# Kernel optimization log

Measured on AMD Instinct MI355X. Metric: run time of the kernel, lower is better.

## Reference

```python
import jax, jax.numpy as jnp
import numpy as np

B, N, D, H = 16, 512, 256, 8
DK = D // H
EPS = 1e-6
NEG_INF = 1e12
LAM_ATT, LAM_DIST, LAM_ADJ = 0.3, 0.3, 0.4


def setup_inputs() -> dict:
    key = jax.random.key(0)
    ks = jax.random.split(key, 16)
    inp = {
        "query": jax.random.normal(ks[0], (B, N, D), jnp.float32),
        "key": jax.random.normal(ks[1], (B, N, D), jnp.float32),
        "value": jax.random.normal(ks[2], (B, N, D), jnp.float32),
        "adj_matrix": jax.random.uniform(ks[3], (B, N, N), jnp.float32),
        "distances_matrix": jax.random.uniform(ks[4], (B, N, N), jnp.float32),
        "edges_att": jnp.zeros((1,), jnp.float32),
        "mask": jnp.ones((B, N), jnp.int32),
    }
    s = 1.0 / np.sqrt(D)
    # four Linear(d_model, d_model): Wq, Wk, Wv, Wo (+ biases)
    for i, nm in enumerate(["q", "k", "v", "o"]):
        inp[f"W{nm}"] = jax.random.normal(ks[5 + 2 * i], (D, D), jnp.float32) * s
        inp[f"b{nm}"] = jax.random.normal(ks[6 + 2 * i], (D,), jnp.float32) * s
    return inp


def _proj(x, W, b):
    # [B,N,D] -> [B,H,N,DK]
    y = x @ W.T + b
    return y.reshape(B, N, H, DK).transpose(0, 2, 1, 3)


def reference(query, key, value, adj_matrix, distances_matrix, edges_att, mask,
              Wq, bq, Wk, bk, Wv, bv, Wo, bo):
    q = _proj(query, Wq, bq)
    k = _proj(key, Wk, bk)
    v = _proj(value, Wv, bv)

    valid = mask != 0  # [B,N] key-side validity

    # distance kernel: softmax(-d) over keys, masked positions -> 0 prob
    d_scores = jnp.where(valid[:, None, :], -distances_matrix, -jnp.inf)
    p_dist = jax.nn.softmax(d_scores, axis=-1)  # [B,N,N]

    # scaled dot-product attention with key mask
    scores = jnp.einsum("bhqd,bhkd->bhqk", q, k) / np.sqrt(DK)
    scores = jnp.where(valid[:, None, None, :], scores, -NEG_INF)
    p_attn = jax.nn.softmax(scores, axis=-1)  # [B,H,N,N]

    # row-normalized adjacency
    p_adj = adj_matrix / (adj_matrix.sum(axis=-1, keepdims=True) + EPS)  # [B,N,N]

    # blend three attention terms (broadcast dist/adj over heads)
    p_weighted = (LAM_ATT * p_attn
                  + LAM_DIST * p_dist[:, None]
                  + LAM_ADJ * p_adj[:, None])  # [B,H,N,N]

    x = jnp.einsum("bhqk,bhkd->bhqd", p_weighted, v)  # [B,H,N,DK]
    x = x.transpose(0, 2, 1, 3).reshape(B, N, D)
    out = x @ Wo.T + bo  # output projection (4th linear)
    return out
```

## Files before the change

### kernel.cpp

```cpp
#include <hip/hip_runtime.h>
#include <cstdint>
#include <cstddef>

#define B_  16
#define N_  512
#define D_  256
#define H_  8
#define DK_ 32

#define QKV_ELEMS 2097152

__device__ __align__(16) unsigned short g_Qb[QKV_ELEMS];
__device__ __align__(16) unsigned short g_Kb[QKV_ELEMS];
__device__ __align__(16) unsigned short g_VT[QKV_ELEMS];
__device__ __align__(16) unsigned short g_WoB[D_*D_];

typedef short v8s __attribute__((ext_vector_type(8)));
typedef float v4f __attribute__((ext_vector_type(4)));

__device__ __forceinline__ unsigned short f2b(float f){
  unsigned int x;
  __builtin_memcpy(&x, &f, 4);
  x = x + 0x7FFFu + ((x >> 16) & 1u);
  return (unsigned short)(x >> 16);
}
__device__ __forceinline__ v8s pack8(const float4 a, const float4 b){
  v8s o;
  o[0]=(short)f2b(a.x); o[1]=(short)f2b(a.y); o[2]=(short)f2b(a.z); o[3]=(short)f2b(a.w);
  o[4]=(short)f2b(b.x); o[5]=(short)f2b(b.y); o[6]=(short)f2b(b.z); o[7]=(short)f2b(b.w);
  return o;
}

__global__ __launch_bounds__(256) void fused_pre(
    const float* __restrict__ query, const float* __restrict__ key_,
    const float* __restrict__ value,
    const float* __restrict__ Wq, const float* __restrict__ bq,
    const float* __restrict__ Wk, const float* __restrict__ bk,
    const float* __restrict__ Wv, const float* __restrict__ bv,
    const float* __restrict__ Wo)
{
  __shared__ unsigned short Wl[64*264];
  const int bid = blockIdx.x;
  const int t   = threadIdx.x;

  if (bid >= 1536){
    const int i = ((bid - 1536)*256 + t)*4;
    const float4 u = *reinterpret_cast<const float4*>(Wo + i);
    ushort4 o4;
    o4.x = f2b(u.x); o4.y = f2b(u.y); o4.z = f2b(u.z); o4.w = f2b(u.w);
    *reinterpret_cast<ushort4*>(g_WoB + i) = o4;
    return;
  }

  const int z  = bid >> 9;
  const int rr = bid & 511;
  const int mt = rr >> 2, nt = rr & 3;
  const float* Ap = (z==0) ? query : (z==1) ? key_ : value;
  const float* Wp = (z==0) ? Wq : (z==1) ? Wk : Wv;
  const float* bp = (z==0) ? bq : (z==1) ? bk : bv;
  const int w = t >> 6, lane = t & 63, kl = lane & 15, quad = lane >> 4;
  const int m0 = mt*64 + w*16;
  const int n0 = nt*64;

  {
    const int row = t >> 2;
    const int ks  = (t & 3) * 64;
    const float* src = Wp + (size_t)(n0+row)*256 + ks;
    unsigned short* dst = Wl + row*264 + ks;
    #pragma unroll
    for (int u = 0; u < 8; ++u){
      const float4 u0 = reinterpret_cast<const float4*>(src)[2*u];
      const float4 u1 = reinterpret_cast<const float4*>(src)[2*u+1];
      *reinterpret_cast<v8s*>(dst + u*8) = pack8(u0, u1);
    }
  }
  __syncthreads();

  v4f acc[4];
  #pragma unroll
  for (int nb = 0; nb < 4; ++nb) acc[nb] = (v4f){0.f,0.f,0.f,0.f};
  const int arow = m0 + kl;

  if (z == 2){
    #pragma unroll
    for (int k0 = 0; k0 < 256; k0 += 32){
      const float* ap = Ap + (size_t)arow*256 + k0 + quad*8;
      const v8s af = pack8(reinterpret_cast<const float4*>(ap)[0],
                           reinterpret_cast<const float4*>(ap)[1]);
      #pragma unroll
      for (int nb = 0; nb < 4; ++nb){
        const v8s wf = *reinterpret_cast<const v8s*>(&Wl[(nb*16+kl)*264 + k0 + quad*8]);
        acc[nb] = __builtin_amdgcn_mfma_f32_16x16x32_bf16(wf, af, acc[nb], 0, 0, 0);
      }
    }
    const int tok = m0 + kl, bb = tok >> 9, nr = tok & 511;
    #pragma unroll
    for (int nb = 0; nb < 4; ++nb)
      #pragma unroll
      for (int r = 0; r < 4; ++r){
        const int n = n0 + nb*16 + quad*4 + r;
        const float v = acc[nb][r] + bp[n];
        g_VT[(((size_t)bb*H_ + (n>>5))*DK_ + (n&31))*N_ + nr] = f2b(v);
      }
  } else {
    #pragma unroll
    for (int k0 = 0; k0 < 256; k0 += 32){
      const float* ap = Ap + (size_t)arow*256 + k0 + quad*8;
      const v8s af = pack8(reinterpret_cast<const float4*>(ap)[0],
                           reinterpret_cast<const float4*>(ap)[1]);
      #pragma unroll
      for (int nb = 0; nb < 4; ++nb){
        const v8s wf = *reinterpret_cast<const v8s*>(&Wl[(nb*16+kl)*264 + k0 + quad*8]);
        acc[nb] = __builtin_amdgcn_mfma_f32_16x16x32_bf16(af, wf, acc[nb], 0, 0, 0);
      }
    }
    unsigned short* dst = z ? g_Kb : g_Qb;
    #pragma unroll
    for (int nb = 0; nb < 4; ++nb){
      const int n = n0 + nb*16 + kl;
      const float bias = bp[n];
      #pragma unroll
      for (int r = 0; r < 4; ++r){
        const int m = m0 + quad*4 + r;
        const float v = acc[nb][r] + bias;
        dst[(((size_t)(m>>9)*H_ + (n>>5))*N_ + (m&511))*DK_ + (n&31)] = f2b(v);
      }
    }
  }
}

__global__ __launch_bounds__(512) void attn_kernel(
    const float* __restrict__ dist, const float* __restrict__ adjm,
    const int* __restrict__ mask,   const float* __restrict__ bo,
    float* __restrict__ out)
{
  __shared__ unsigned short STl[16*520];
  __shared__ unsigned short Pl[8*16*40];
  __shared__ unsigned short Xl[16*272];
  const int bid = blockIdx.x;
  const int b  = bid & 15;
  const int qt = bid >> 4;
  const int q0 = qt*16;
  const int t  = threadIdx.x;
  const int w  = t >> 6, lane = t & 63;
  const int kl = lane & 15, quad = lane >> 4;

  {
    const int row = t >> 5;
    const int seg = t & 31;
    const size_t roff = ((size_t)(b*N_ + q0 + row))*N_ + seg*16;
    float dv[16], av[16]; int mk[16];
    #pragma unroll
    for (int c = 0; c < 4; ++c){
      const float4 d4 = *reinterpret_cast<const float4*>(dist + roff + c*4);
      const float4 a4 = *reinterpret_cast<const float4*>(adjm + roff + c*4);
      const int4   m4 = *reinterpret_cast<const int4*>(mask + b*N_ + seg*16 + c*4);
      dv[c*4+0]=d4.x; dv[c*4+1]=d4.y; dv[c*4+2]=d4.z; dv[c*4+3]=d4.w;
      av[c*4+0]=a4.x; av[c*4+1]=a4.y; av[c*4+2]=a4.z; av[c*4+3]=a4.w;
      mk[c*4+0]=m4.x; mk[c*4+1]=m4.y; mk[c*4+2]=m4.z; mk[c*4+3]=m4.w;
    }
    float ev[16], lz = 0.f, la = 0.f;
    #pragma unroll
    for (int i = 0; i < 16; ++i){
      ev[i] = mk[i] ? __expf(-dv[i]) : 0.f;
      lz += ev[i];
      la += av[i];
    }
    #pragma unroll
    for (int o = 1; o < 32; o <<= 1){
      lz += __shfl_xor(lz, o, 64);
      la += __shfl_xor(la, o, 64);
    }
    const float c0 = (lz > 0.f) ? 0.3f / lz : 0.f;
    const float c1 = 0.4f / (la + 1e-6f);
    v8s s0, s1;
    #pragma unroll
    for (int i = 0; i < 8; ++i){
      s0[i] = (short)f2b(ev[i]*c0   + av[i]*c1);
      s1[i] = (short)f2b(ev[8+i]*c0 + av[8+i]*c1);
    }
    *reinterpret_cast<v8s*>(&STl[row*520 + seg*16])     = s0;
    *reinterpret_cast<v8s*>(&STl[row*520 + seg*16 + 8]) = s1;
  }
  __syncthreads();

  {
    const int h = w;
    const size_t bh = (size_t)b*H_ + h;
    const float scale = 0.17677669529663687f;
    const unsigned short* Qp = g_Qb + (bh*N_ + q0)*DK_;
    const unsigned short* Kp = g_Kb + bh*N_*DK_;
    const unsigned short* Vp = g_VT + bh*DK_*N_;
    unsigned short* Plw = Pl + w*640;
    const v8s aq = *reinterpret_cast<const v8s*>(Qp + (size_t)kl*DK_ + quad*8);
    const v4f vz = {0.f, 0.f, 0.f, 0.f};

    v4f acc[32];
    #pragma unroll
    for (int kb = 0; kb < 32; ++kb){
      const v8s bk = *reinterpret_cast<const v8s*>(Kp + (size_t)(kb*16 + kl)*DK_ + quad*8);
      acc[kb] = __builtin_amdgcn_mfma_f32_16x16x32_bf16(aq, bk, vz, 0, 0, 0);
    }

    const int* mrow = mask + b*N_;
    float lsum[4] = {0.f, 0.f, 0.f, 0.f};
    #pragma unroll
    for (int kb = 0; kb < 32; ++kb){
      const bool valid = (mrow[kb*16 + kl] != 0);
      #pragma unroll
      for (int r = 0; r < 4; ++r){
        const float e = valid ? __expf(acc[kb][r]*scale) : 0.f;
        acc[kb][r] = e;
        lsum[r] += e;
      }
    }
    #pragma unroll
    for (int r = 0; r < 4; ++r)
      #pragma unroll
      for (int o = 1; o < 16; o <<= 1) lsum[r] += __shfl_xor(lsum[r], o, 64);
    float inv[4];
    #pragma unroll
    for (int r = 0; r < 4; ++r) inv[r] = (lsum[r] > 0.f) ? 0.3f / lsum[r] : 0.f;

    v4f o0 = vz, o1 = vz;
    #pragma unroll
    for (int c = 0; c < 16; ++c){
      #pragma unroll
      for (int r = 0; r < 4; ++r){
        Plw[(quad*4 + r)*40 + kl]      = f2b(acc[2*c    ][r] * inv[r]);
        Plw[(quad*4 + r)*40 + 16 + kl] = f2b(acc[2*c + 1][r] * inv[r]);
      }
      const v8s bp  = *reinterpret_cast<const v8s*>(&Plw[kl*40 + quad*8]);
      const v8s bst = *reinterpret_cast<const v8s*>(&STl[kl*520 + c*32 + quad*8]);
      const v8s av0 = *reinterpret_cast<const v8s*>(Vp + (size_t)(     kl)*N_ + c*32 + quad*8);
      const v8s av1 = *reinterpret_cast<const v8s*>(Vp + (size_t)(16 + kl)*N_ + c*32 + quad*8);
      o0 = __builtin_amdgcn_mfma_f32_16x16x32_bf16(av0, bp,  o0, 0, 0, 0);
      o0 = __builtin_amdgcn_mfma_f32_16x16x32_bf16(av0, bst, o0, 0, 0, 0);
      o1 = __builtin_amdgcn_mfma_f32_16x16x32_bf16(av1, bp,  o1, 0, 0, 0);
      o1 = __builtin_amdgcn_mfma_f32_16x16x32_bf16(av1, bst, o1, 0, 0, 0);
    }

    unsigned short* xr = Xl + kl*272 + h*32;
    #pragma unroll
    for (int r = 0; r < 4; ++r){
      xr[     quad*4 + r] = f2b(o0[r]);
      xr[16 + quad*4 + r] = f2b(o1[r]);
    }
  }
  __syncthreads();

  {
    const int n0 = w*32;
    v4f a2[2];
    a2[0] = (v4f){0.f,0.f,0.f,0.f};
    a2[1] = (v4f){0.f,0.f,0.f,0.f};
    #pragma unroll
    for (int k0 = 0; k0 < 256; k0 += 32){
      const v8s af = *reinterpret_cast<const v8s*>(&Xl[kl*272 + k0 + quad*8]);
      #pragma unroll
      for (int nb = 0; nb < 2; ++nb){
        const v8s wf = *reinterpret_cast<const v8s*>(
            g_WoB + (size_t)(n0 + nb*16 + kl)*256 + k0 + quad*8);
        a2[nb] = __builtin_amdgcn_mfma_f32_16x16x32_bf16(af, wf, a2[nb], 0, 0, 0);
      }
    }
    #pragma unroll
    for (int nb = 0; nb < 2; ++nb){
      const int n = n0 + nb*16 + kl;
      const float bias = bo[n];
      #pragma unroll
      for (int r = 0; r < 4; ++r)
        out[((size_t)(b*N_ + q0 + quad*4 + r))*256 + n] = a2[nb][r] + bias;
    }
  }
}

extern "C" void kernel_launch(void* const* d_in, const int* in_sizes, int n_in,
                              void* d_out, int out_size, void* d_ws, size_t ws_size,
                              hipStream_t stream)
{
  const float* query = (const float*)d_in[0];
  const float* key_  = (const float*)d_in[1];
  const float* value = (const float*)d_in[2];
  const float* adjm  = (const float*)d_in[3];
  const float* dist  = (const float*)d_in[4];
  const int*   mask  = (const int*)d_in[6];
  const float* Wq = (const float*)d_in[7];  const float* bq = (const float*)d_in[8];
  const float* Wk = (const float*)d_in[9];  const float* bk = (const float*)d_in[10];
  const float* Wv = (const float*)d_in[11]; const float* bv = (const float*)d_in[12];
  const float* Wo = (const float*)d_in[13]; const float* bo = (const float*)d_in[14];

  fused_pre<<<1600, 256, 0, stream>>>(query, key_, value,
                                      Wq, bq, Wk, bk, Wv, bv, Wo);
  attn_kernel<<<512, 512, 0, stream>>>(dist, adjm, mask, bo, (float*)d_out);
}
```

Measured before the change: 181.5 us.

## Precompute dist/adj blend in pre-kernel and chunk attention with deferred normalization

Measured after the change: 180.4 us. No clear change (-0.6%).

```diff
diff --git a/kernel.cpp b/kernel.cpp
--- a/kernel.cpp
+++ b/kernel.cpp
@@ -14,6 +14,7 @@
 __device__ __align__(16) unsigned short g_Kb[QKV_ELEMS];
 __device__ __align__(16) unsigned short g_VT[QKV_ELEMS];
 __device__ __align__(16) unsigned short g_WoB[D_*D_];
+__device__ __align__(16) unsigned short g_ST[B_*N_*N_];
 
 typedef short v8s __attribute__((ext_vector_type(8)));
 typedef float v4f __attribute__((ext_vector_type(4)));
@@ -37,23 +38,70 @@
     const float* __restrict__ Wq, const float* __restrict__ bq,
     const float* __restrict__ Wk, const float* __restrict__ bk,
     const float* __restrict__ Wv, const float* __restrict__ bv,
-    const float* __restrict__ Wo)
+    const float* __restrict__ Wo,
+    const float* __restrict__ dist, const float* __restrict__ adjm,
+    const int* __restrict__ mask)
 {
   __shared__ unsigned short Wl[64*264];
   const int bid = blockIdx.x;
   const int t   = threadIdx.x;
 
-  if (bid >= 1536){
-    const int i = ((bid - 1536)*256 + t)*4;
+  if (bid < 512){
+    const int b   = bid & 15;
+    const int qt  = bid >> 4;
+    const int row = t >> 4;
+    const int seg = t & 15;
+    const size_t roff = ((size_t)(b*N_ + qt*16 + row))*N_ + seg*32;
+    const float* dp = dist + roff;
+    const float* ap = adjm + roff;
+    const int*   mp = mask + b*N_ + seg*32;
+    float ev[32], av[32];
+    float lz = 0.f, la = 0.f;
+    #pragma unroll
+    for (int c = 0; c < 8; ++c){
+      const float4 d4 = *reinterpret_cast<const float4*>(dp + c*4);
+      const float4 a4 = *reinterpret_cast<const float4*>(ap + c*4);
+      const int4   m4 = *reinterpret_cast<const int4*>(mp + c*4);
+      ev[c*4+0] = m4.x ? __expf(-d4.x) : 0.f;
+      ev[c*4+1] = m4.y ? __expf(-d4.y) : 0.f;
+      ev[c*4+2] = m4.z ? __expf(-d4.z) : 0.f;
+      ev[c*4+3] = m4.w ? __expf(-d4.w) : 0.f;
+      av[c*4+0] = a4.x; av[c*4+1] = a4.y; av[c*4+2] = a4.z; av[c*4+3] = a4.w;
+      lz += ev[c*4+0] + ev[c*4+1] + ev[c*4+2] + ev[c*4+3];
+      la += a4.x + a4.y + a4.z + a4.w;
+    }
+    #pragma unroll
+    for (int o = 1; o < 16; o <<= 1){
+      lz += __shfl_xor(lz, o, 64);
+      la += __shfl_xor(la, o, 64);
+    }
+    const float c0 = (lz > 0.f) ? 0.3f / lz : 0.f;
+    const float c1 = 0.4f / (la + 1e-6f);
+    unsigned short* dst = g_ST + roff;
+    #pragma unroll
+    for (int c2 = 0; c2 < 4; ++c2){
+      v8s o8;
+      #pragma unroll
+      for (int i = 0; i < 8; ++i)
+        o8[i] = (short)f2b(ev[c2*8+i]*c0 + av[c2*8+i]*c1);
+      *reinterpret_cast<v8s*>(dst + c2*8) = o8;
+    }
+    return;
+  }
+
+  if (bid >= 2048){
+    const int i = ((bid - 2048)*256 + t)*4;
     const float4 u = *reinterpret_cast<const float4*>(Wo + i);
+    const int n = i >> 8, k = i & 255;
     ushort4 o4;
     o4.x = f2b(u.x); o4.y = f2b(u.y); o4.z = f2b(u.z); o4.w = f2b(u.w);
-    *reinterpret_cast<ushort4*>(g_WoB + i) = o4;
+    *reinterpret_cast<ushort4*>(g_WoB + (size_t)(k >> 5)*8192 + (size_t)n*32 + (k & 31)) = o4;
     return;
   }
 
-  const int z  = bid >> 9;
-  const int rr = bid & 511;
+  const int gb = bid - 512;
+  const int z  = gb >> 9;
+  const int rr = gb & 511;
   const int mt = rr >> 2, nt = rr & 3;
   const float* Ap = (z==0) ? query : (z==1) ? key_ : value;
   const float* Wp = (z==0) ? Wq : (z==1) ? Wk : Wv;
@@ -100,7 +148,7 @@
       for (int r = 0; r < 4; ++r){
         const int n = n0 + nb*16 + quad*4 + r;
         const float v = acc[nb][r] + bp[n];
-        g_VT[(((size_t)bb*H_ + (n>>5))*DK_ + (n&31))*N_ + nr] = f2b(v);
+        g_VT[(((size_t)bb*H_ + (n>>5))*16 + (nr>>5))*1024 + (size_t)(n&31)*32 + (nr&31)] = f2b(v);
       }
   } else {
     #pragma unroll
@@ -129,9 +177,8 @@
   }
 }
 
-__global__ __launch_bounds__(512) void attn_kernel(
-    const float* __restrict__ dist, const float* __restrict__ adjm,
-    const int* __restrict__ mask,   const float* __restrict__ bo,
+__global__ __launch_bounds__(512, 4) void attn_kernel(
+    const int* __restrict__ mask, const float* __restrict__ bo,
     float* __restrict__ out)
 {
   __shared__ unsigned short STl[16*520];
@@ -147,66 +194,41 @@
 
   {
     const int row = t >> 5;
-    const int seg = t & 31;
-    const size_t roff = ((size_t)(b*N_ + q0 + row))*N_ + seg*16;
-    float dv[16], av[16]; int mk[16];
-    #pragma unroll
-    for (int c = 0; c < 4; ++c){
-      const float4 d4 = *reinterpret_cast<const float4*>(dist + roff + c*4);
-      const float4 a4 = *reinterpret_cast<const float4*>(adjm + roff + c*4);
-      const int4   m4 = *reinterpret_cast<const int4*>(mask + b*N_ + seg*16 + c*4);
-      dv[c*4+0]=d4.x; dv[c*4+1]=d4.y; dv[c*4+2]=d4.z; dv[c*4+3]=d4.w;
-      av[c*4+0]=a4.x; av[c*4+1]=a4.y; av[c*4+2]=a4.z; av[c*4+3]=a4.w;
-      mk[c*4+0]=m4.x; mk[c*4+1]=m4.y; mk[c*4+2]=m4.z; mk[c*4+3]=m4.w;
-    }
-    float ev[16], lz = 0.f, la = 0.f;
-    #pragma unroll
-    for (int i = 0; i < 16; ++i){
-      ev[i] = mk[i] ? __expf(-dv[i]) : 0.f;
-      lz += ev[i];
-      la += av[i];
-    }
-    #pragma unroll
-    for (int o = 1; o < 32; o <<= 1){
-      lz += __shfl_xor(lz, o, 64);
-      la += __shfl_xor(la, o, 64);
-    }
-    const float c0 = (lz > 0.f) ? 0.3f / lz : 0.f;
-    const float c1 = 0.4f / (la + 1e-6f);
-    v8s s0, s1;
-    #pragma unroll
-    for (int i = 0; i < 8; ++i){
-      s0[i] = (short)f2b(ev[i]*c0   + av[i]*c1);
-      s1[i] = (short)f2b(ev[8+i]*c0 + av[8+i]*c1);
-    }
-    *reinterpret_cast<v8s*>(&STl[row*520 + seg*16])     = s0;
-    *reinterpret_cast<v8s*>(&STl[row*520 + seg*16 + 8]) = s1;
-  }
+    const int c16 = (t & 31) * 16;
+    const unsigned short* src = g_ST + ((size_t)(b*N_ + q0 + row))*N_ + c16;
+    *reinterpret_cast<v8s*>(&STl[row*520 + c16])     = *reinterpret_cast<const v8s*>(src);
+    *reinterpret_cast<v8s*>(&STl[row*520 + c16 + 8]) = *reinterpret_cast<const v8s*>(src + 8);
+  }
+
+  const int h = w;
+  const size_t bh = (size_t)b*H_ + h;
+  const float scale = 0.17677669529663687f;
+  const unsigned short* Qp = g_Qb + (bh*N_ + q0)*DK_;
+  const unsigned short* Kp = g_Kb + bh*N_*DK_;
+  const unsigned short* Vp = g_VT + bh*(size_t)(N_*DK_);
+  unsigned short* Plw = Pl + w*640;
+  const int* mrow = mask + b*N_;
+  const v8s aq = *reinterpret_cast<const v8s*>(Qp + (size_t)kl*DK_ + quad*8);
+  const v4f vz = {0.f, 0.f, 0.f, 0.f};
+
+  v4f oA0 = vz, oA1 = vz;
+  v4f oS0 = vz, oS1 = vz;
+  float lsum[4] = {0.f, 0.f, 0.f, 0.f};
+
   __syncthreads();
 
-  {
-    const int h = w;
-    const size_t bh = (size_t)b*H_ + h;
-    const float scale = 0.17677669529663687f;
-    const unsigned short* Qp = g_Qb + (bh*N_ + q0)*DK_;
-    const unsigned short* Kp = g_Kb + bh*N_*DK_;
-    const unsigned short* Vp = g_VT + bh*DK_*N_;
-    unsigned short* Plw = Pl + w*640;
-    const v8s aq = *reinterpret_cast<const v8s*>(Qp + (size_t)kl*DK_ + quad*8);
-    const v4f vz = {0.f, 0.f, 0.f, 0.f};
-
-    v4f acc[32];
-    #pragma unroll
-    for (int kb = 0; kb < 32; ++kb){
-      const v8s bk = *reinterpret_cast<const v8s*>(Kp + (size_t)(kb*16 + kl)*DK_ + quad*8);
+  #pragma unroll 1
+  for (int ch = 0; ch < 4; ++ch){
+    const int k0 = ch*128;
+    v4f acc[8];
+    #pragma unroll
+    for (int kb = 0; kb < 8; ++kb){
+      const v8s bk = *reinterpret_cast<const v8s*>(Kp + (size_t)(k0 + kb*16 + kl)*DK_ + quad*8);
       acc[kb] = __builtin_amdgcn_mfma_f32_16x16x32_bf16(aq, bk, vz, 0, 0, 0);
     }
-
-    const int* mrow = mask + b*N_;
-    float lsum[4] = {0.f, 0.f, 0.f, 0.f};
-    #pragma unroll
-    for (int kb = 0; kb < 32; ++kb){
-      const bool valid = (mrow[kb*16 + kl] != 0);
+    #pragma unroll
+    for (int kb = 0; kb < 8; ++kb){
+      const bool valid = (mrow[k0 + kb*16 + kl] != 0);
       #pragma unroll
       for (int r = 0; r < 4; ++r){
         const float e = valid ? __expf(acc[kb][r]*scale) : 0.f;
@@ -215,52 +237,53 @@
       }
     }
     #pragma unroll
-    for (int r = 0; r < 4; ++r)
-      #pragma unroll
-      for (int o = 1; o < 16; o <<= 1) lsum[r] += __shfl_xor(lsum[r], o, 64);
-    float inv[4];
-    #pragma unroll
-    for (int r = 0; r < 4; ++r) inv[r] = (lsum[r] > 0.f) ? 0.3f / lsum[r] : 0.f;
-
-    v4f o0 = vz, o1 = vz;
-    #pragma unroll
-    for (int c = 0; c < 16; ++c){
+    for (int cc = 0; cc < 4; ++cc){
       #pragma unroll
       for (int r = 0; r < 4; ++r){
-        Plw[(quad*4 + r)*40 + kl]      = f2b(acc[2*c    ][r] * inv[r]);
-        Plw[(quad*4 + r)*40 + 16 + kl] = f2b(acc[2*c + 1][r] * inv[r]);
-      }
+        Plw[(quad*4 + r)*40 + kl]      = f2b(acc[2*cc    ][r]);
+        Plw[(quad*4 + r)*40 + 16 + kl] = f2b(acc[2*cc + 1][r]);
+      }
+      const int kk = k0 + cc*32;
       const v8s bp  = *reinterpret_cast<const v8s*>(&Plw[kl*40 + quad*8]);
-      const v8s bst = *reinterpret_cast<const v8s*>(&STl[kl*520 + c*32 + quad*8]);
-      const v8s av0 = *reinterpret_cast<const v8s*>(Vp + (size_t)(     kl)*N_ + c*32 + quad*8);
-      const v8s av1 = *reinterpret_cast<const v8s*>(Vp + (size_t)(16 + kl)*N_ + c*32 + quad*8);
-      o0 = __builtin_amdgcn_mfma_f32_16x16x32_bf16(av0, bp,  o0, 0, 0, 0);
-      o0 = __builtin_amdgcn_mfma_f32_16x16x32_bf16(av0, bst, o0, 0, 0, 0);
-      o1 = __builtin_amdgcn_mfma_f32_16x16x32_bf16(av1, bp,  o1, 0, 0, 0);
-      o1 = __builtin_amdgcn_mfma_f32_16x16x32_bf16(av1, bst, o1, 0, 0, 0);
-    }
-
-    unsigned short* xr = Xl + kl*272 + h*32;
-    #pragma unroll
-    for (int r = 0; r < 4; ++r){
-      xr[     quad*4 + r] = f2b(o0[r]);
-      xr[16 + quad*4 + r] = f2b(o1[r]);
-    }
+      const v8s bst = *reinterpret_cast<const v8s*>(&STl[kl*520 + kk + quad*8]);
+      const v8s av0 = *reinterpret_cast<const v8s*>(Vp + (size_t)(kk + kl)*32 + quad*8);
+      const v8s av1 = *reinterpret_cast<const v8s*>(Vp + (size_t)(kk + 16 + kl)*32 + quad*8);
+      oA0 = __builtin_amdgcn_mfma_f32_16x16x32_bf16(av0, bp,  oA0, 0, 0, 0);
+      oS0 = __builtin_amdgcn_mfma_f32_16x16x32_bf16(av0, bst, oS0, 0, 0, 0);
+      oA1 = __builtin_amdgcn_mfma_f32_16x16x32_bf16(av1, bp,  oA1, 0, 0, 0);
+      oS1 = __builtin_amdgcn_mfma_f32_16x16x32_bf16(av1, bst, oS1, 0, 0, 0);
+    }
+  }
+
+  #pragma unroll
+  for (int r = 0; r < 4; ++r)
+    #pragma unroll
+    for (int o = 1; o < 16; o <<= 1) lsum[r] += __shfl_xor(lsum[r], o, 64);
+  const float s01 = (kl & 1) ? lsum[1] : lsum[0];
+  const float s23 = (kl & 1) ? lsum[3] : lsum[2];
+  const float sv  = (kl & 2) ? s23 : s01;
+  float inv = __shfl(sv, ((kl >> 2) << 4) | (kl & 3), 64);
+  inv = (inv > 0.f) ? 0.3f / inv : 0.f;
+
+  unsigned short* xr = Xl + kl*272 + h*32;
+  #pragma unroll
+  for (int r = 0; r < 4; ++r){
+    xr[     quad*4 + r] = f2b(oA0[r]*inv + oS0[r]);
+    xr[16 + quad*4 + r] = f2b(oA1[r]*inv + oS1[r]);
   }
   __syncthreads();
 
   {
     const int n0 = w*32;
     v4f a2[2];
-    a2[0] = (v4f){0.f,0.f,0.f,0.f};
-    a2[1] = (v4f){0.f,0.f,0.f,0.f};
+    a2[0] = vz; a2[1] = vz;
     #pragma unroll
     for (int k0 = 0; k0 < 256; k0 += 32){
       const v8s af = *reinterpret_cast<const v8s*>(&Xl[kl*272 + k0 + quad*8]);
       #pragma unroll
       for (int nb = 0; nb < 2; ++nb){
         const v8s wf = *reinterpret_cast<const v8s*>(
-            g_WoB + (size_t)(n0 + nb*16 + kl)*256 + k0 + quad*8);
+            g_WoB + (size_t)(k0 >> 5)*8192 + (size_t)(n0 + nb*16 + kl)*32 + quad*8);
         a2[nb] = __builtin_amdgcn_mfma_f32_16x16x32_bf16(af, wf, a2[nb], 0, 0, 0);
       }
     }
@@ -290,7 +313,8 @@
   const float* Wv = (const float*)d_in[11]; const float* bv = (const float*)d_in[12];
   const float* Wo = (const float*)d_in[13]; const float* bo = (const float*)d_in[14];
 
-  fused_pre<<<1600, 256, 0, stream>>>(query, key_, value,
-                                      Wq, bq, Wk, bk, Wv, bv, Wo);
-  attn_kernel<<<512, 512, 0, stream>>>(dist, adjm, mask, bo, (float*)d_out);
-}
+  fused_pre<<<2112, 256, 0, stream>>>(query, key_, value,
+                                      Wq, bq, Wk, bk, Wv, bv, Wo,
+                                      dist, adjm, mask);
+  attn_kernel<<<512, 512, 0, stream>>>(mask, bo, (float*)d_out);
+}
```
